# Kernel tuning notes

Hardware: AMD Instinct MI355X
Metric: run time of the kernel (lower is better)

## Reference

```python
import jax, jax.numpy as jnp
import numpy as np

H = 24  # hidden size hard-coded in TrendGRU


def setup_inputs() -> dict:
    key = jax.random.key(0)
    ks = jax.random.split(key, 7)
    B, T = 32768, 512
    s_ih = 1.0 / np.sqrt(H)
    x = jax.random.normal(ks[0], (B, T, 1), dtype=jnp.float32)
    # GRUCell params (PyTorch layout: rows ordered r, z, n)
    W_ih = jax.random.uniform(ks[1], (3 * H, 1), minval=-s_ih, maxval=s_ih, dtype=jnp.float32)
    W_hh = jax.random.uniform(ks[2], (3 * H, H), minval=-s_ih, maxval=s_ih, dtype=jnp.float32)
    b_ih = jax.random.uniform(ks[3], (3 * H,), minval=-s_ih, maxval=s_ih, dtype=jnp.float32)
    b_hh = jax.random.uniform(ks[4], (3 * H,), minval=-s_ih, maxval=s_ih, dtype=jnp.float32)
    fc_w = jax.random.uniform(ks[5], (2, H), minval=-s_ih, maxval=s_ih, dtype=jnp.float32)
    fc_b = jax.random.uniform(ks[6], (2,), minval=-s_ih, maxval=s_ih, dtype=jnp.float32)
    return {"x": x, "W_ih": W_ih, "b_ih": b_ih, "W_hh": W_hh, "b_hh": b_hh,
            "fc_w": fc_w, "fc_b": fc_b}


def _gru_scan(x, W_ih, b_ih, W_hh, b_hh):
    B = x.shape[0]
    # precompute input projections for all timesteps: (B,T,1)@(1,3H) -> (T,B,3H)
    gx = jnp.einsum('bti,gi->tbg', x, W_ih) + b_ih
    h0 = jnp.zeros((B, H), dtype=x.dtype)

    def step(h, gx_t):
        gh = h @ W_hh.T + b_hh                      # (B, 3H)
        xr, xz, xn = jnp.split(gx_t, 3, axis=-1)    # PyTorch order r, z, n
        hr, hz, hn = jnp.split(gh, 3, axis=-1)
        r = jax.nn.sigmoid(xr + hr)
        z = jax.nn.sigmoid(xz + hz)
        n = jnp.tanh(xn + r * hn)
        h_new = (1.0 - z) * n + z * h
        return h_new, None

    h_final, _ = jax.lax.scan(step, h0, gx)
    return h_final


def reference(x, W_ih, b_ih, W_hh, b_hh, fc_w, fc_b):
    h = _gru_scan(x, W_ih, b_ih, W_hh, b_hh)
    return h @ fc_w.T + fc_b  # (B, 2)
```

## Files before the change

kernel.cpp:

```cpp
#include <hip/hip_runtime.h>


#define GRU_T 512
#define FS 28

typedef __attribute__((ext_vector_type(8)))  short bf16x8;
typedef __attribute__((ext_vector_type(16))) float f32x16;
typedef __attribute__((ext_vector_type(2)))  float f32x2;
typedef __attribute__((ext_vector_type(2)))  unsigned uint2v;

__device__ __forceinline__ float bf16hi_f(float v) {
    unsigned u = __float_as_uint(v);
    u = (u + 0x7FFFu + ((u >> 16) & 1u)) & 0xFFFF0000u;
    return __uint_as_float(u);
}
__device__ __forceinline__ unsigned bf16_rne(float v) {
    unsigned u = __float_as_uint(v);
    return (u + 0x7FFFu + ((u >> 16) & 1u)) >> 16;
}
__device__ __forceinline__ unsigned cvt_pk_bf16(float lo, float hi) {
    unsigned r;
    asm("v_cvt_pk_bf16_f32 %0, %1, %2" : "=v"(r) : "v"(lo), "v"(hi));
    return r;
}
__device__ __forceinline__ f32x16 mfma32(bf16x8 a, bf16x8 b, f32x16 c) {
    return __builtin_amdgcn_mfma_f32_32x32x16_bf16(a, b, c, 0, 0, 0);
}

__device__ __forceinline__ unsigned pair_epi(float ar0, float ar1,
                                             float az0, float az1,
                                             float an0, float an1,
                                             const f32x2 aX, f32x2& h)
{
    const f32x2 one2 = {1.0f, 1.0f};
    f32x2 er2, ez2, ev2;
    er2.x = __builtin_amdgcn_exp2f(-ar0);
    er2.y = __builtin_amdgcn_exp2f(-ar1);
    ez2.x = __builtin_amdgcn_exp2f(-az0);
    ez2.y = __builtin_amdgcn_exp2f(-az1);
    const f32x2 dr2 = er2 + one2;
    const f32x2 dz2 = ez2 + one2;
    const f32x2 pp2 = dr2 * dz2;
    const float  Q  = __builtin_amdgcn_rcpf(pp2.x * pp2.y);
    f32x2 qi2; qi2.x = Q * pp2.y; qi2.y = Q * pp2.x;
    const f32x2 rr2 = qi2 * dz2;
    const f32x2 zz2 = qi2 * dr2;
    const f32x2 an2 = {an0, an1};
    const f32x2 u2  = __builtin_elementwise_fma(rr2, an2, aX);
    ev2.x = __builtin_amdgcn_exp2f(u2.x);
    ev2.y = __builtin_amdgcn_exp2f(u2.y);
    const f32x2 dv2 = ev2 + one2;
    const float  Qn = __builtin_amdgcn_rcpf(dv2.x * dv2.y);
    f32x2 rv2; rv2.x = Qn * dv2.y; rv2.y = Qn * dv2.x;
    const f32x2 m2  = {-2.0f, -2.0f};
    const f32x2 nn2 = __builtin_elementwise_fma(m2, rv2, one2);
    const f32x2 hm2 = h - nn2;
    const f32x2 hn2 = __builtin_elementwise_fma(zz2, hm2, nn2);
    h = hn2;
    return cvt_pk_bf16(hn2.x, hn2.y);
}

__global__ __launch_bounds__(64) void trend_gru_mfma32(
    const float* __restrict__ x,
    const float* __restrict__ W_ih,
    const float* __restrict__ b_ih,
    const float* __restrict__ W_hh,
    const float* __restrict__ b_hh,
    const float* __restrict__ fc_w,
    const float* __restrict__ fc_b,
    float* __restrict__ out)
{
    const int lane = threadIdx.x;
    const int e    = lane & 31;
    const int half = lane >> 5;
    const int elem0 = blockIdx.x * 32;

    __shared__ __align__(16) float Flds[32 * FS];

    const float L2E = 1.4426950408889634f;

    bf16x8 A[3][2][2];
#pragma unroll
    for (int g = 0; g < 3; ++g) {
        const float sc = (g == 2) ? 2.0f * L2E : L2E;
        const int m = e;
        const bool valid = m < 24;
        const int R = g * 24 + (valid ? m : 0);
        const float wx = (g < 2 && valid) ? sc * W_ih[R] : 0.0f;
        const float bb = valid ? sc * ((g < 2) ? (b_ih[R] + b_hh[R]) : b_hh[R]) : 0.0f;
        const float wxh = bf16hi_f(wx), bbh = bf16hi_f(bb);
#pragma unroll
        for (int s = 0; s < 2; ++s) {
            bf16x8 fh, fl;
#pragma unroll
            for (int jj = 0; jj < 8; ++jj) {
                const int k = s * 16 + half * 8 + jj;
                float vh = 0.0f, vl = 0.0f;
                if (valid && k < 24) {
                    const float w  = sc * W_hh[R * 24 + k];
                    const float wh = bf16hi_f(w);
                    vh = wh; vl = w - wh;
                } else if (valid) {
                    if (k == 24 || k == 25)      vh = wxh;
                    else if (k == 26)            vh = wx - wxh;
                    else if (k == 27)            vh = bbh;
                    else if (k == 28)            vh = bb - bbh;
                }
                fh[jj] = (short)bf16_rne(vh);
                fl[jj] = (short)bf16_rne(vl);
            }
            A[g][s][0] = fh;
            A[g][s][1] = fl;
        }
    }

    f32x2 wn2[6], bn2[6];
#pragma unroll
    for (int p = 0; p < 6; ++p) {
#pragma unroll
        for (int c = 0; c < 2; ++c) {
            const int s = p * 2 + c;
            const int j = (s & 3) + 8 * (s >> 2) + 4 * half;
            wn2[p][c] = 2.0f * L2E * W_ih[48 + j];
            bn2[p][c] = 2.0f * L2E * b_ih[48 + j];
        }
    }

    const float* xp = x + (size_t)(elem0 + e) * GRU_T;

    f32x2 h2[6];
#pragma unroll
    for (int p = 0; p < 6; ++p) { h2[p].x = 0.0f; h2[p].y = 0.0f; }

    const f32x16 z16 = {0.f,0.f,0.f,0.f,0.f,0.f,0.f,0.f,
                        0.f,0.f,0.f,0.f,0.f,0.f,0.f,0.f};

    float xv    = xp[0];
    float xnext = xp[1];

    f32x2 aX2[6];
#pragma unroll
    for (int p = 0; p < 6; ++p) {
        const f32x2 xb = {xv, xv};
        aX2[p] = __builtin_elementwise_fma(wn2[p], xb, bn2[p]);
    }

    f32x16 aR, aZ, aN;
    {
        uint4 b1q; b1q.x = 0u; b1q.y = 0u; b1q.z = 0u; b1q.w = 0u;
        if (half) {
            const unsigned xy = cvt_pk_bf16(xv, 1.0f);
            const float    xh = __uint_as_float(xy << 16);
            const unsigned xx = cvt_pk_bf16(xv, xv - xh);
            b1q.x = xx; b1q.y = xy; b1q.z = 0x00003F80u; b1q.w = 0u;
        }
        const bf16x8 B1 = *(const bf16x8*)&b1q;
        uint4 b0q; b0q.x = 0u; b0q.y = 0u; b0q.z = 0u; b0q.w = 0u;
        const bf16x8 B0 = *(const bf16x8*)&b0q;
        aR = mfma32(A[0][1][0], B1, mfma32(A[0][1][1], B1, z16));
        aZ = mfma32(A[1][1][0], B1, mfma32(A[1][1][1], B1, z16));
        aN = mfma32(A[2][1][0], B1, mfma32(A[2][1][1], B1, z16));
        aR = mfma32(A[0][0][0], B0, mfma32(A[0][0][1], B0, aR));
        aZ = mfma32(A[1][0][0], B0, mfma32(A[1][0][1], B0, aZ));
        aN = mfma32(A[2][0][0], B0, mfma32(A[2][0][1], B0, aN));
    }

#pragma unroll 1
    for (int t = 0; t < GRU_T - 1; ++t) {
        const unsigned nP4 = pair_epi(aR[8],  aR[9],  aZ[8],  aZ[9],
                                      aN[8],  aN[9],  aX2[4], h2[4]);
        const unsigned nP5 = pair_epi(aR[10], aR[11], aZ[10], aZ[11],
                                      aN[10], aN[11], aX2[5], h2[5]);
        const uint2v r44 = __builtin_amdgcn_permlane32_swap(nP4, nP4, false, false);
        const uint2v r55 = __builtin_amdgcn_permlane32_swap(nP5, nP5, false, false);
        uint4 b1q;
        b1q.x = nP4;
        b1q.y = nP5;
        b1q.z = r44.y;
        b1q.w = r55.y;
        if (half) {
            const unsigned xy = cvt_pk_bf16(xnext, 1.0f);
            const float    xh = __uint_as_float(xy << 16);
            const unsigned xx = cvt_pk_bf16(xnext, xnext - xh);
            b1q.x = xx; b1q.y = xy; b1q.z = 0x00003F80u; b1q.w = 0u;
        }
        const bf16x8 B1 = *(const bf16x8*)&b1q;

        f32x16 nR = mfma32(A[0][1][0], B1, mfma32(A[0][1][1], B1, z16));
        f32x16 nZ = mfma32(A[1][1][0], B1, mfma32(A[1][1][1], B1, z16));
        f32x16 nN = mfma32(A[2][1][0], B1, mfma32(A[2][1][1], B1, z16));

        const unsigned nP0 = pair_epi(aR[0], aR[1], aZ[0], aZ[1],
                                      aN[0], aN[1], aX2[0], h2[0]);
        const unsigned nP1 = pair_epi(aR[2], aR[3], aZ[2], aZ[3],
                                      aN[2], aN[3], aX2[1], h2[1]);
        const unsigned nP2 = pair_epi(aR[4], aR[5], aZ[4], aZ[5],
                                      aN[4], aN[5], aX2[2], h2[2]);
        const unsigned nP3 = pair_epi(aR[6], aR[7], aZ[6], aZ[7],
                                      aN[6], aN[7], aX2[3], h2[3]);
        const uint2v r02 = __builtin_amdgcn_permlane32_swap(nP0, nP2, false, false);
        const uint2v r13 = __builtin_amdgcn_permlane32_swap(nP1, nP3, false, false);
        uint4 b0q;
        b0q.x = r02.x;
        b0q.y = r13.x;
        b0q.z = r02.y;
        b0q.w = r13.y;
        const bf16x8 B0 = *(const bf16x8*)&b0q;

        nR = mfma32(A[0][0][0], B0, mfma32(A[0][0][1], B0, nR));
        nZ = mfma32(A[1][0][0], B0, mfma32(A[1][0][1], B0, nZ));
        nN = mfma32(A[2][0][0], B0, mfma32(A[2][0][1], B0, nN));

        const float xcur = xnext;
        xnext = xp[(t + 2 < GRU_T) ? t + 2 : GRU_T - 1];
#pragma unroll
        for (int p = 0; p < 6; ++p) {
            const f32x2 xb = {xcur, xcur};
            aX2[p] = __builtin_elementwise_fma(wn2[p], xb, bn2[p]);
        }
        aR = nR; aZ = nZ; aN = nN;
    }

    (void)pair_epi(aR[8],  aR[9],  aZ[8],  aZ[9],  aN[8],  aN[9],  aX2[4], h2[4]);
    (void)pair_epi(aR[10], aR[11], aZ[10], aZ[11], aN[10], aN[11], aX2[5], h2[5]);
    (void)pair_epi(aR[0],  aR[1],  aZ[0],  aZ[1],  aN[0],  aN[1],  aX2[0], h2[0]);
    (void)pair_epi(aR[2],  aR[3],  aZ[2],  aZ[3],  aN[2],  aN[3],  aX2[1], h2[1]);
    (void)pair_epi(aR[4],  aR[5],  aZ[4],  aZ[5],  aN[4],  aN[5],  aX2[2], h2[2]);
    (void)pair_epi(aR[6],  aR[7],  aZ[6],  aZ[7],  aN[6],  aN[7],  aX2[3], h2[3]);

#pragma unroll
    for (int G = 0; G < 3; ++G) {
        float4 f4;
        f4.x = h2[G * 2 + 0].x; f4.y = h2[G * 2 + 0].y;
        f4.z = h2[G * 2 + 1].x; f4.w = h2[G * 2 + 1].y;
        *(float4*)(&Flds[e * FS + G * 8 + half * 4]) = f4;
    }
    __builtin_amdgcn_s_barrier();
    if (lane < 32) {
        float o0 = fc_b[0], o1 = fc_b[1];
#pragma unroll
        for (int j = 0; j < 24; ++j) {
            const float hv = Flds[lane * FS + j];
            o0 = fmaf(hv, fc_w[j],      o0);
            o1 = fmaf(hv, fc_w[24 + j], o1);
        }
        float2 o; o.x = o0; o.y = o1;
        *(float2*)(out + (size_t)(elem0 + lane) * 2) = o;
    }
}

extern "C" void kernel_launch(void* const* d_in, const int* in_sizes, int n_in,
                              void* d_out, int out_size, void* d_ws, size_t ws_size,
                              hipStream_t stream) {
    const float* x    = (const float*)d_in[0];
    const float* W_ih = (const float*)d_in[1];
    const float* b_ih = (const float*)d_in[2];
    const float* W_hh = (const float*)d_in[3];
    const float* b_hh = (const float*)d_in[4];
    const float* fc_w = (const float*)d_in[5];
    const float* fc_b = (const float*)d_in[6];
    float* out = (float*)d_out;

    const int B = in_sizes[0] / GRU_T;
    const int grid = B / 32;
    trend_gru_mfma32<<<grid, 64, 0, stream>>>(x, W_ih, b_ih, W_hh, b_hh,
                                              fc_w, fc_b, out);
}
```

Measured before the change: 454.0 us.

## Switch GRU recurrence from 32x32 MFMA to 16x16x32 MFMA with 16 sequences per wave

```diff
diff --git a/kernel.cpp b/kernel.cpp
--- a/kernel.cpp
+++ b/kernel.cpp
@@ -5,9 +5,8 @@
 #define FS 28
 
 typedef __attribute__((ext_vector_type(8)))  short bf16x8;
-typedef __attribute__((ext_vector_type(16))) float f32x16;
+typedef __attribute__((ext_vector_type(4)))  float f32x4;
 typedef __attribute__((ext_vector_type(2)))  float f32x2;
-typedef __attribute__((ext_vector_type(2)))  unsigned uint2v;
 
 __device__ __forceinline__ float bf16hi_f(float v) {
     unsigned u = __float_as_uint(v);
@@ -23,8 +22,8 @@
     asm("v_cvt_pk_bf16_f32 %0, %1, %2" : "=v"(r) : "v"(lo), "v"(hi));
     return r;
 }
-__device__ __forceinline__ f32x16 mfma32(bf16x8 a, bf16x8 b, f32x16 c) {
-    return __builtin_amdgcn_mfma_f32_32x32x16_bf16(a, b, c, 0, 0, 0);
+__device__ __forceinline__ f32x4 mfma16(bf16x8 a, bf16x8 b, f32x4 c) {
+    return __builtin_amdgcn_mfma_f32_16x16x32_bf16(a, b, c, 0, 0, 0);
 }
 
 __device__ __forceinline__ unsigned pair_epi(float ar0, float ar1,
@@ -60,7 +59,7 @@
     return cvt_pk_bf16(hn2.x, hn2.y);
 }
 
-__global__ __launch_bounds__(64) void trend_gru_mfma32(
+__global__ __launch_bounds__(64) void trend_gru_mfma16(
     const float* __restrict__ x,
     const float* __restrict__ W_ih,
     const float* __restrict__ b_ih,
@@ -71,30 +70,30 @@
     float* __restrict__ out)
 {
     const int lane = threadIdx.x;
-    const int e    = lane & 31;
-    const int half = lane >> 5;
-    const int elem0 = blockIdx.x * 32;
-
-    __shared__ __align__(16) float Flds[32 * FS];
+    const int e = lane & 15;
+    const int g = lane >> 4;
+    const int elem0 = blockIdx.x * 16;
+
+    __shared__ __align__(16) float Flds[16 * FS];
 
     const float L2E = 1.4426950408889634f;
 
     bf16x8 A[3][2][2];
 #pragma unroll
-    for (int g = 0; g < 3; ++g) {
-        const float sc = (g == 2) ? 2.0f * L2E : L2E;
-        const int m = e;
-        const bool valid = m < 24;
-        const int R = g * 24 + (valid ? m : 0);
-        const float wx = (g < 2 && valid) ? sc * W_ih[R] : 0.0f;
-        const float bb = valid ? sc * ((g < 2) ? (b_ih[R] + b_hh[R]) : b_hh[R]) : 0.0f;
-        const float wxh = bf16hi_f(wx), bbh = bf16hi_f(bb);
-#pragma unroll
-        for (int s = 0; s < 2; ++s) {
+    for (int gate = 0; gate < 3; ++gate) {
+        const float sc = (gate == 2) ? 2.0f * L2E : L2E;
+#pragma unroll
+        for (int tile = 0; tile < 2; ++tile) {
+            const int m = tile * 16 + e;
+            const bool valid = m < 24;
+            const int R = gate * 24 + (valid ? m : 0);
+            const float wx = (gate < 2 && valid) ? sc * W_ih[R] : 0.0f;
+            const float bb = valid ? sc * ((gate < 2) ? (b_ih[R] + b_hh[R]) : b_hh[R]) : 0.0f;
+            const float wxh = bf16hi_f(wx), bbh = bf16hi_f(bb);
             bf16x8 fh, fl;
 #pragma unroll
-            for (int jj = 0; jj < 8; ++jj) {
-                const int k = s * 16 + half * 8 + jj;
+            for (int i = 0; i < 8; ++i) {
+                const int k = g * 8 + i;
                 float vh = 0.0f, vl = 0.0f;
                 if (valid && k < 24) {
                     const float w  = sc * W_hh[R * 24 + k];
@@ -106,137 +105,105 @@
                     else if (k == 27)            vh = bbh;
                     else if (k == 28)            vh = bb - bbh;
                 }
-                fh[jj] = (short)bf16_rne(vh);
-                fl[jj] = (short)bf16_rne(vl);
+                fh[i] = (short)bf16_rne(vh);
+                fl[i] = (short)bf16_rne(vl);
             }
-            A[g][s][0] = fh;
-            A[g][s][1] = fl;
-        }
-    }
-
-    f32x2 wn2[6], bn2[6];
-#pragma unroll
-    for (int p = 0; p < 6; ++p) {
+            A[gate][tile][0] = fh;
+            A[gate][tile][1] = fl;
+        }
+    }
+
+    f32x2 wn2[4], bn2[4];
+#pragma unroll
+    for (int p = 0; p < 4; ++p) {
 #pragma unroll
         for (int c = 0; c < 2; ++c) {
-            const int s = p * 2 + c;
-            const int j = (s & 3) + 8 * (s >> 2) + 4 * half;
+            int j = (p < 2) ? (4 * g + 2 * p + c) : (16 + 4 * g + 2 * (p - 2) + c);
+            if (j > 23) j = 23;
             wn2[p][c] = 2.0f * L2E * W_ih[48 + j];
             bn2[p][c] = 2.0f * L2E * b_ih[48 + j];
         }
     }
 
     const float* xp = x + (size_t)(elem0 + e) * GRU_T;
-
-    f32x2 h2[6];
-#pragma unroll
-    for (int p = 0; p < 6; ++p) { h2[p].x = 0.0f; h2[p].y = 0.0f; }
-
-    const f32x16 z16 = {0.f,0.f,0.f,0.f,0.f,0.f,0.f,0.f,
-                        0.f,0.f,0.f,0.f,0.f,0.f,0.f,0.f};
-
-    float xv    = xp[0];
-    float xnext = xp[1];
-
-    f32x2 aX2[6];
-#pragma unroll
-    for (int p = 0; p < 6; ++p) {
+    float xv = xp[0];
+
+    f32x2 h2[4];
+#pragma unroll
+    for (int p = 0; p < 4; ++p) { h2[p].x = 0.0f; h2[p].y = 0.0f; }
+
+    f32x2 aX2[4];
+#pragma unroll
+    for (int p = 0; p < 4; ++p) {
         const f32x2 xb = {xv, xv};
         aX2[p] = __builtin_elementwise_fma(wn2[p], xb, bn2[p]);
     }
 
-    f32x16 aR, aZ, aN;
+    unsigned Wd0 = 0, Wd1 = 0, Wd2 = 0, Wd3 = 0;
+
+    const int idxA = (e + ((g & 1) << 5)) << 2;
+    const int idxB = idxA + (16 << 2);
+    const int idxC = e << 2;
+    const int idxD = (e + 16) << 2;
+    const bool mg2 = (g == 2);
+    const bool mg3 = (g == 3);
+
+    const f32x4 z4 = {0.f, 0.f, 0.f, 0.f};
+
+#pragma unroll 1
+    for (int t = 0; t < GRU_T; ++t) {
+        const unsigned xy = cvt_pk_bf16(xv, 1.0f);
+        const float    xh = __uint_as_float(xy << 16);
+        const unsigned xx = cvt_pk_bf16(xv, xv - xh);
+
+        unsigned Bd0 = (unsigned)__builtin_amdgcn_ds_bpermute(idxA, (int)Wd0);
+        unsigned Bd1 = (unsigned)__builtin_amdgcn_ds_bpermute(idxA, (int)Wd1);
+        unsigned Bd2 = (unsigned)__builtin_amdgcn_ds_bpermute(idxB, (int)Wd0);
+        unsigned Bd3 = (unsigned)__builtin_amdgcn_ds_bpermute(idxB, (int)Wd1);
+        const unsigned c0 = (unsigned)__builtin_amdgcn_ds_bpermute(idxC, (int)Wd2);
+        const unsigned c1 = (unsigned)__builtin_amdgcn_ds_bpermute(idxC, (int)Wd3);
+        const unsigned c2 = (unsigned)__builtin_amdgcn_ds_bpermute(idxD, (int)Wd2);
+        const unsigned c3 = (unsigned)__builtin_amdgcn_ds_bpermute(idxD, (int)Wd3);
+        Bd0 = mg2 ? c0 : Bd0;  Bd1 = mg2 ? c1 : Bd1;
+        Bd2 = mg2 ? c2 : Bd2;  Bd3 = mg2 ? c3 : Bd3;
+        Bd0 = mg3 ? xx : Bd0;  Bd1 = mg3 ? xy : Bd1;
+        Bd2 = mg3 ? 0x00003F80u : Bd2;  Bd3 = mg3 ? 0u : Bd3;
+        uint4 bq; bq.x = Bd0; bq.y = Bd1; bq.z = Bd2; bq.w = Bd3;
+        const bf16x8 Bf = *(const bf16x8*)&bq;
+        const float xnext = xp[(t + 1 < GRU_T) ? t + 1 : t];
+
+        f32x4 cR0 = mfma16(A[0][0][0], Bf, z4); cR0 = mfma16(A[0][0][1], Bf, cR0);
+        f32x4 cZ0 = mfma16(A[1][0][0], Bf, z4); cZ0 = mfma16(A[1][0][1], Bf, cZ0);
+        f32x4 cN0 = mfma16(A[2][0][0], Bf, z4); cN0 = mfma16(A[2][0][1], Bf, cN0);
+        f32x4 cR1 = mfma16(A[0][1][0], Bf, z4); cR1 = mfma16(A[0][1][1], Bf, cR1);
+        f32x4 cZ1 = mfma16(A[1][1][0], Bf, z4); cZ1 = mfma16(A[1][1][1], Bf, cZ1);
+        f32x4 cN1 = mfma16(A[2][1][0], Bf, z4); cN1 = mfma16(A[2][1][1], Bf, cN1);
+
+        Wd0 = pair_epi(cR0[0], cR0[1], cZ0[0], cZ0[1], cN0[0], cN0[1], aX2[0], h2[0]);
+        Wd1 = pair_epi(cR0[2], cR0[3], cZ0[2], cZ0[3], cN0[2], cN0[3], aX2[1], h2[1]);
+        Wd2 = pair_epi(cR1[0], cR1[1], cZ1[0], cZ1[1], cN1[0], cN1[1], aX2[2], h2[2]);
+        Wd3 = pair_epi(cR1[2], cR1[3], cZ1[2], cZ1[3], cN1[2], cN1[3], aX2[3], h2[3]);
+
+        xv = xnext;
+#pragma unroll
+        for (int p = 0; p < 4; ++p) {
+            const f32x2 xb = {xv, xv};
+            aX2[p] = __builtin_elementwise_fma(wn2[p], xb, bn2[p]);
+        }
+    }
+
     {
-        uint4 b1q; b1q.x = 0u; b1q.y = 0u; b1q.z = 0u; b1q.w = 0u;
-        if (half) {
-            const unsigned xy = cvt_pk_bf16(xv, 1.0f);
-            const float    xh = __uint_as_float(xy << 16);
-            const unsigned xx = cvt_pk_bf16(xv, xv - xh);
-            b1q.x = xx; b1q.y = xy; b1q.z = 0x00003F80u; b1q.w = 0u;
-        }
-        const bf16x8 B1 = *(const bf16x8*)&b1q;
-        uint4 b0q; b0q.x = 0u; b0q.y = 0u; b0q.z = 0u; b0q.w = 0u;
-        const bf16x8 B0 = *(const bf16x8*)&b0q;
-        aR = mfma32(A[0][1][0], B1, mfma32(A[0][1][1], B1, z16));
-        aZ = mfma32(A[1][1][0], B1, mfma32(A[1][1][1], B1, z16));
-        aN = mfma32(A[2][1][0], B1, mfma32(A[2][1][1], B1, z16));
-        aR = mfma32(A[0][0][0], B0, mfma32(A[0][0][1], B0, aR));
-        aZ = mfma32(A[1][0][0], B0, mfma32(A[1][0][1], B0, aZ));
-        aN = mfma32(A[2][0][0], B0, mfma32(A[2][0][1], B0, aN));
-    }
-
-#pragma unroll 1
-    for (int t = 0; t < GRU_T - 1; ++t) {
-        const unsigned nP4 = pair_epi(aR[8],  aR[9],  aZ[8],  aZ[9],
-                                      aN[8],  aN[9],  aX2[4], h2[4]);
-        const unsigned nP5 = pair_epi(aR[10], aR[11], aZ[10], aZ[11],
-                                      aN[10], aN[11], aX2[5], h2[5]);
-        const uint2v r44 = __builtin_amdgcn_permlane32_swap(nP4, nP4, false, false);
-        const uint2v r55 = __builtin_amdgcn_permlane32_swap(nP5, nP5, false, false);
-        uint4 b1q;
-        b1q.x = nP4;
-        b1q.y = nP5;
-        b1q.z = r44.y;
-        b1q.w = r55.y;
-        if (half) {
-            const unsigned xy = cvt_pk_bf16(xnext, 1.0f);
-            const float    xh = __uint_as_float(xy << 16);
-            const unsigned xx = cvt_pk_bf16(xnext, xnext - xh);
-            b1q.x = xx; b1q.y = xy; b1q.z = 0x00003F80u; b1q.w = 0u;
-        }
-        const bf16x8 B1 = *(const bf16x8*)&b1q;
-
-        f32x16 nR = mfma32(A[0][1][0], B1, mfma32(A[0][1][1], B1, z16));
-        f32x16 nZ = mfma32(A[1][1][0], B1, mfma32(A[1][1][1], B1, z16));
-        f32x16 nN = mfma32(A[2][1][0], B1, mfma32(A[2][1][1], B1, z16));
-
-        const unsigned nP0 = pair_epi(aR[0], aR[1], aZ[0], aZ[1],
-                                      aN[0], aN[1], aX2[0], h2[0]);
-        const unsigned nP1 = pair_epi(aR[2], aR[3], aZ[2], aZ[3],
-                                      aN[2], aN[3], aX2[1], h2[1]);
-        const unsigned nP2 = pair_epi(aR[4], aR[5], aZ[4], aZ[5],
-                                      aN[4], aN[5], aX2[2], h2[2]);
-        const unsigned nP3 = pair_epi(aR[6], aR[7], aZ[6], aZ[7],
-                                      aN[6], aN[7], aX2[3], h2[3]);
-        const uint2v r02 = __builtin_amdgcn_permlane32_swap(nP0, nP2, false, false);
-        const uint2v r13 = __builtin_amdgcn_permlane32_swap(nP1, nP3, false, false);
-        uint4 b0q;
-        b0q.x = r02.x;
-        b0q.y = r13.x;
-        b0q.z = r02.y;
-        b0q.w = r13.y;
-        const bf16x8 B0 = *(const bf16x8*)&b0q;
-
-        nR = mfma32(A[0][0][0], B0, mfma32(A[0][0][1], B0, nR));
-        nZ = mfma32(A[1][0][0], B0, mfma32(A[1][0][1], B0, nZ));
-        nN = mfma32(A[2][0][0], B0, mfma32(A[2][0][1], B0, nN));
-
-        const float xcur = xnext;
-        xnext = xp[(t + 2 < GRU_T) ? t + 2 : GRU_T - 1];
-#pragma unroll
-        for (int p = 0; p < 6; ++p) {
-            const f32x2 xb = {xcur, xcur};
-            aX2[p] = __builtin_elementwise_fma(wn2[p], xb, bn2[p]);
-        }
-        aR = nR; aZ = nZ; aN = nN;
-    }
-
-    (void)pair_epi(aR[8],  aR[9],  aZ[8],  aZ[9],  aN[8],  aN[9],  aX2[4], h2[4]);
-    (void)pair_epi(aR[10], aR[11], aZ[10], aZ[11], aN[10], aN[11], aX2[5], h2[5]);
-    (void)pair_epi(aR[0],  aR[1],  aZ[0],  aZ[1],  aN[0],  aN[1],  aX2[0], h2[0]);
-    (void)pair_epi(aR[2],  aR[3],  aZ[2],  aZ[3],  aN[2],  aN[3],  aX2[1], h2[1]);
-    (void)pair_epi(aR[4],  aR[5],  aZ[4],  aZ[5],  aN[4],  aN[5],  aX2[2], h2[2]);
-    (void)pair_epi(aR[6],  aR[7],  aZ[6],  aZ[7],  aN[6],  aN[7],  aX2[3], h2[3]);
-
-#pragma unroll
-    for (int G = 0; G < 3; ++G) {
         float4 f4;
-        f4.x = h2[G * 2 + 0].x; f4.y = h2[G * 2 + 0].y;
-        f4.z = h2[G * 2 + 1].x; f4.w = h2[G * 2 + 1].y;
-        *(float4*)(&Flds[e * FS + G * 8 + half * 4]) = f4;
+        f4.x = h2[0].x; f4.y = h2[0].y; f4.z = h2[1].x; f4.w = h2[1].y;
+        *(float4*)(&Flds[e * FS + 4 * g]) = f4;
+        if (g < 2) {
+            float4 f5;
+            f5.x = h2[2].x; f5.y = h2[2].y; f5.z = h2[3].x; f5.w = h2[3].y;
+            *(float4*)(&Flds[e * FS + 16 + 4 * g]) = f5;
+        }
     }
     __builtin_amdgcn_s_barrier();
-    if (lane < 32) {
+    if (lane < 16) {
         float o0 = fc_b[0], o1 = fc_b[1];
 #pragma unroll
         for (int j = 0; j < 24; ++j) {
@@ -262,7 +229,7 @@
     float* out = (float*)d_out;
 
     const int B = in_sizes[0] / GRU_T;
-    const int grid = B / 32;
-    trend_gru_mfma32<<<grid, 64, 0, stream>>>(x, W_ih, b_ih, W_hh, b_hh,
+    const int grid = B / 16;
+    trend_gru_mfma16<<<grid, 64, 0, stream>>>(x, W_ih, b_ih, W_hh, b_hh,
                                               fc_w, fc_b, out);
 }
```

Result: slower. 514.5 us (+13.3%).

## Interleave two independent GRU sequences per wave to hide MFMA latency

Applied to the files above, without the earlier changes.

```diff
diff --git a/kernel.cpp b/kernel.cpp
--- a/kernel.cpp
+++ b/kernel.cpp
@@ -60,7 +60,7 @@
     return cvt_pk_bf16(hn2.x, hn2.y);
 }
 
-__global__ __launch_bounds__(64) void trend_gru_mfma32(
+__global__ __launch_bounds__(64, 1) void trend_gru_dual(
     const float* __restrict__ x,
     const float* __restrict__ W_ih,
     const float* __restrict__ b_ih,
@@ -73,9 +73,9 @@
     const int lane = threadIdx.x;
     const int e    = lane & 31;
     const int half = lane >> 5;
-    const int elem0 = blockIdx.x * 32;
-
-    __shared__ __align__(16) float Flds[32 * FS];
+    const int elem0 = blockIdx.x * 64;
+
+    __shared__ __align__(16) float Flds[2 * 32 * FS];
 
     const float L2E = 1.4426950408889634f;
 
@@ -126,126 +126,169 @@
         }
     }
 
-    const float* xp = x + (size_t)(elem0 + e) * GRU_T;
-
-    f32x2 h2[6];
-#pragma unroll
-    for (int p = 0; p < 6; ++p) { h2[p].x = 0.0f; h2[p].y = 0.0f; }
+    const float* xpa = x + (size_t)(elem0 + e) * GRU_T;
+    const float* xpb = xpa + (size_t)32 * GRU_T;
+
+    f32x2 h2a[6], h2b[6];
+#pragma unroll
+    for (int p = 0; p < 6; ++p) {
+        h2a[p].x = 0.0f; h2a[p].y = 0.0f;
+        h2b[p].x = 0.0f; h2b[p].y = 0.0f;
+    }
+    unsigned Pa0 = 0, Pa1 = 0, Pa2 = 0, Pa3 = 0, Pa4 = 0, Pa5 = 0;
+    unsigned Pb0 = 0, Pb1 = 0, Pb2 = 0, Pb3 = 0, Pb4 = 0, Pb5 = 0;
+
+    float xva = xpa[0];
+    float xvb = xpb[0];
+
+    f32x2 aX2a[6], aX2b[6];
+#pragma unroll
+    for (int p = 0; p < 6; ++p) {
+        const f32x2 xa = {xva, xva};
+        const f32x2 xb = {xvb, xvb};
+        aX2a[p] = __builtin_elementwise_fma(wn2[p], xa, bn2[p]);
+        aX2b[p] = __builtin_elementwise_fma(wn2[p], xb, bn2[p]);
+    }
 
     const f32x16 z16 = {0.f,0.f,0.f,0.f,0.f,0.f,0.f,0.f,
                         0.f,0.f,0.f,0.f,0.f,0.f,0.f,0.f};
 
-    float xv    = xp[0];
-    float xnext = xp[1];
-
-    f32x2 aX2[6];
-#pragma unroll
-    for (int p = 0; p < 6; ++p) {
-        const f32x2 xb = {xv, xv};
-        aX2[p] = __builtin_elementwise_fma(wn2[p], xb, bn2[p]);
-    }
-
-    f32x16 aR, aZ, aN;
-    {
-        uint4 b1q; b1q.x = 0u; b1q.y = 0u; b1q.z = 0u; b1q.w = 0u;
+#pragma unroll 1
+    for (int t = 0; t < GRU_T; ++t) {
+        const uint2v ra02 = __builtin_amdgcn_permlane32_swap(Pa0, Pa2, false, false);
+        const uint2v ra13 = __builtin_amdgcn_permlane32_swap(Pa1, Pa3, false, false);
+        uint4 b0qa;
+        b0qa.x = ra02.x; b0qa.y = ra13.x; b0qa.z = ra02.y; b0qa.w = ra13.y;
+        const uint2v ra44 = __builtin_amdgcn_permlane32_swap(Pa4, Pa4, false, false);
+        const uint2v ra55 = __builtin_amdgcn_permlane32_swap(Pa5, Pa5, false, false);
+        uint4 b1qa;
+        b1qa.x = Pa4; b1qa.y = Pa5; b1qa.z = ra44.y; b1qa.w = ra55.y;
         if (half) {
-            const unsigned xy = cvt_pk_bf16(xv, 1.0f);
+            const unsigned xy = cvt_pk_bf16(xva, 1.0f);
             const float    xh = __uint_as_float(xy << 16);
-            const unsigned xx = cvt_pk_bf16(xv, xv - xh);
-            b1q.x = xx; b1q.y = xy; b1q.z = 0x00003F80u; b1q.w = 0u;
-        }
-        const bf16x8 B1 = *(const bf16x8*)&b1q;
-        uint4 b0q; b0q.x = 0u; b0q.y = 0u; b0q.z = 0u; b0q.w = 0u;
-        const bf16x8 B0 = *(const bf16x8*)&b0q;
-        aR = mfma32(A[0][1][0], B1, mfma32(A[0][1][1], B1, z16));
-        aZ = mfma32(A[1][1][0], B1, mfma32(A[1][1][1], B1, z16));
-        aN = mfma32(A[2][1][0], B1, mfma32(A[2][1][1], B1, z16));
-        aR = mfma32(A[0][0][0], B0, mfma32(A[0][0][1], B0, aR));
-        aZ = mfma32(A[1][0][0], B0, mfma32(A[1][0][1], B0, aZ));
-        aN = mfma32(A[2][0][0], B0, mfma32(A[2][0][1], B0, aN));
-    }
-
-#pragma unroll 1
-    for (int t = 0; t < GRU_T - 1; ++t) {
-        const unsigned nP4 = pair_epi(aR[8],  aR[9],  aZ[8],  aZ[9],
-                                      aN[8],  aN[9],  aX2[4], h2[4]);
-        const unsigned nP5 = pair_epi(aR[10], aR[11], aZ[10], aZ[11],
-                                      aN[10], aN[11], aX2[5], h2[5]);
-        const uint2v r44 = __builtin_amdgcn_permlane32_swap(nP4, nP4, false, false);
-        const uint2v r55 = __builtin_amdgcn_permlane32_swap(nP5, nP5, false, false);
-        uint4 b1q;
-        b1q.x = nP4;
-        b1q.y = nP5;
-        b1q.z = r44.y;
-        b1q.w = r55.y;
+            const unsigned xx = cvt_pk_bf16(xva, xva - xh);
+            b1qa.x = xx; b1qa.y = xy; b1qa.z = 0x00003F80u; b1qa.w = 0u;
+        }
+        const bf16x8 B0a = *(const bf16x8*)&b0qa;
+        const bf16x8 B1a = *(const bf16x8*)&b1qa;
+        const float xnexta = xpa[(t + 1 < GRU_T) ? t + 1 : t];
+
+        f32x16 aRa = mfma32(A[0][0][0], B0a, z16);
+        aRa = mfma32(A[0][0][1], B0a, aRa);
+        aRa = mfma32(A[0][1][0], B1a, aRa);
+        aRa = mfma32(A[0][1][1], B1a, aRa);
+        f32x16 aZa = mfma32(A[1][0][0], B0a, z16);
+        aZa = mfma32(A[1][0][1], B0a, aZa);
+        aZa = mfma32(A[1][1][0], B1a, aZa);
+        aZa = mfma32(A[1][1][1], B1a, aZa);
+        f32x16 aNa = mfma32(A[2][0][0], B0a, z16);
+        aNa = mfma32(A[2][0][1], B0a, aNa);
+        aNa = mfma32(A[2][1][0], B1a, aNa);
+        aNa = mfma32(A[2][1][1], B1a, aNa);
+
+        const uint2v rb02 = __builtin_amdgcn_permlane32_swap(Pb0, Pb2, false, false);
+        const uint2v rb13 = __builtin_amdgcn_permlane32_swap(Pb1, Pb3, false, false);
+        uint4 b0qb;
+        b0qb.x = rb02.x; b0qb.y = rb13.x; b0qb.z = rb02.y; b0qb.w = rb13.y;
+        const uint2v rb44 = __builtin_amdgcn_permlane32_swap(Pb4, Pb4, false, false);
+        const uint2v rb55 = __builtin_amdgcn_permlane32_swap(Pb5, Pb5, false, false);
+        uint4 b1qb;
+        b1qb.x = Pb4; b1qb.y = Pb5; b1qb.z = rb44.y; b1qb.w = rb55.y;
         if (half) {
-            const unsigned xy = cvt_pk_bf16(xnext, 1.0f);
+            const unsigned xy = cvt_pk_bf16(xvb, 1.0f);
             const float    xh = __uint_as_float(xy << 16);
-            const unsigned xx = cvt_pk_bf16(xnext, xnext - xh);
-            b1q.x = xx; b1q.y = xy; b1q.z = 0x00003F80u; b1q.w = 0u;
-        }
-        const bf16x8 B1 = *(const bf16x8*)&b1q;
-
-        f32x16 nR = mfma32(A[0][1][0], B1, mfma32(A[0][1][1], B1, z16));
-        f32x16 nZ = mfma32(A[1][1][0], B1, mfma32(A[1][1][1], B1, z16));
-        f32x16 nN = mfma32(A[2][1][0], B1, mfma32(A[2][1][1], B1, z16));
-
-        const unsigned nP0 = pair_epi(aR[0], aR[1], aZ[0], aZ[1],
-                                      aN[0], aN[1], aX2[0], h2[0]);
-        const unsigned nP1 = pair_epi(aR[2], aR[3], aZ[2], aZ[3],
-                                      aN[2], aN[3], aX2[1], h2[1]);
-        const unsigned nP2 = pair_epi(aR[4], aR[5], aZ[4], aZ[5],
-                                      aN[4], aN[5], aX2[2], h2[2]);
-        const unsigned nP3 = pair_epi(aR[6], aR[7], aZ[6], aZ[7],
-                                      aN[6], aN[7], aX2[3], h2[3]);
-        const uint2v r02 = __builtin_amdgcn_permlane32_swap(nP0, nP2, false, false);
-        const uint2v r13 = __builtin_amdgcn_permlane32_swap(nP1, nP3, false, false);
-        uint4 b0q;
-        b0q.x = r02.x;
-        b0q.y = r13.x;
-        b0q.z = r02.y;
-        b0q.w = r13.y;
-        const bf16x8 B0 = *(const bf16x8*)&b0q;
-
-        nR = mfma32(A[0][0][0], B0, mfma32(A[0][0][1], B0, nR));
-        nZ = mfma32(A[1][0][0], B0, mfma32(A[1][0][1], B0, nZ));
-        nN = mfma32(A[2][0][0], B0, mfma32(A[2][0][1], B0, nN));
-
-        const float xcur = xnext;
-        xnext = xp[(t + 2 < GRU_T) ? t + 2 : GRU_T - 1];
+            const unsigned xx = cvt_pk_bf16(xvb, xvb - xh);
+            b1qb.x = xx; b1qb.y = xy; b1qb.z = 0x00003F80u; b1qb.w = 0u;
+        }
+        const bf16x8 B0b = *(const bf16x8*)&b0qb;
+        const bf16x8 B1b = *(const bf16x8*)&b1qb;
+        const float xnextb = xpb[(t + 1 < GRU_T) ? t + 1 : t];
+
+        f32x16 aRb = mfma32(A[0][0][0], B0b, z16);
+        aRb = mfma32(A[0][0][1], B0b, aRb);
+        aRb = mfma32(A[0][1][0], B1b, aRb);
+        aRb = mfma32(A[0][1][1], B1b, aRb);
+        f32x16 aZb = mfma32(A[1][0][0], B0b, z16);
+        aZb = mfma32(A[1][0][1], B0b, aZb);
+        aZb = mfma32(A[1][1][0], B1b, aZb);
+        aZb = mfma32(A[1][1][1], B1b, aZb);
+        f32x16 aNb = mfma32(A[2][0][0], B0b, z16);
+        aNb = mfma32(A[2][0][1], B0b, aNb);
+        aNb = mfma32(A[2][1][0], B1b, aNb);
+        aNb = mfma32(A[2][1][1], B1b, aNb);
+
+#pragma unroll
+        for (int G = 0; G < 3; ++G) {
+            const unsigned pa = pair_epi(aRa[G*4+0], aRa[G*4+1],
+                                         aZa[G*4+0], aZa[G*4+1],
+                                         aNa[G*4+0], aNa[G*4+1],
+                                         aX2a[G*2], h2a[G*2]);
+            const unsigned pb = pair_epi(aRa[G*4+2], aRa[G*4+3],
+                                         aZa[G*4+2], aZa[G*4+3],
+                                         aNa[G*4+2], aNa[G*4+3],
+                                         aX2a[G*2+1], h2a[G*2+1]);
+            if (G == 0)      { Pa0 = pa; Pa1 = pb; }
+            else if (G == 1) { Pa2 = pa; Pa3 = pb; }
+            else             { Pa4 = pa; Pa5 = pb; }
+        }
+        xva = xnexta;
 #pragma unroll
         for (int p = 0; p < 6; ++p) {
-            const f32x2 xb = {xcur, xcur};
-            aX2[p] = __builtin_elementwise_fma(wn2[p], xb, bn2[p]);
-        }
-        aR = nR; aZ = nZ; aN = nN;
-    }
-
-    (void)pair_epi(aR[8],  aR[9],  aZ[8],  aZ[9],  aN[8],  aN[9],  aX2[4], h2[4]);
-    (void)pair_epi(aR[10], aR[11], aZ[10], aZ[11], aN[10], aN[11], aX2[5], h2[5]);
-    (void)pair_epi(aR[0],  aR[1],  aZ[0],  aZ[1],  aN[0],  aN[1],  aX2[0], h2[0]);
-    (void)pair_epi(aR[2],  aR[3],  aZ[2],  aZ[3],  aN[2],  aN[3],  aX2[1], h2[1]);
-    (void)pair_epi(aR[4],  aR[5],  aZ[4],  aZ[5],  aN[4],  aN[5],  aX2[2], h2[2]);
-    (void)pair_epi(aR[6],  aR[7],  aZ[6],  aZ[7],  aN[6],  aN[7],  aX2[3], h2[3]);
-
+            const f32x2 xa = {xva, xva};
+            aX2a[p] = __builtin_elementwise_fma(wn2[p], xa, bn2[p]);
+        }
+
+#pragma unroll
+        for (int G = 0; G < 3; ++G) {
+            const unsigned pa = pair_epi(aRb[G*4+0], aRb[G*4+1],
+                                         aZb[G*4+0], aZb[G*4+1],
+                                         aNb[G*4+0], aNb[G*4+1],
+                                         aX2b[G*2], h2b[G*2]);
+            const unsigned pb = pair_epi(aRb[G*4+2], aRb[G*4+3],
+                                         aZb[G*4+2], aZb[G*4+3],
+                                         aNb[G*4+2], aNb[G*4+3],
+                                         aX2b[G*2+1], h2b[G*2+1]);
+            if (G == 0)      { Pb0 = pa; Pb1 = pb; }
+            else if (G == 1) { Pb2 = pa; Pb3 = pb; }
+            else             { Pb4 = pa; Pb5 = pb; }
+        }
+        xvb = xnextb;
+#pragma unroll
+        for (int p = 0; p < 6; ++p) {
+            const f32x2 xb = {xvb, xvb};
+            aX2b[p] = __builtin_elementwise_fma(wn2[p], xb, bn2[p]);
+        }
+    }
+
+    float* Fa = Flds;
+    float* Fb = Flds + 32 * FS;
 #pragma unroll
     for (int G = 0; G < 3; ++G) {
         float4 f4;
-        f4.x = h2[G * 2 + 0].x; f4.y = h2[G * 2 + 0].y;
-        f4.z = h2[G * 2 + 1].x; f4.w = h2[G * 2 + 1].y;
-        *(float4*)(&Flds[e * FS + G * 8 + half * 4]) = f4;
-    }
-    __builtin_amdgcn_s_barrier();
+        f4.x = h2a[G * 2 + 0].x; f4.y = h2a[G * 2 + 0].y;
+        f4.z = h2a[G * 2 + 1].x; f4.w = h2a[G * 2 + 1].y;
+        *(float4*)(&Fa[e * FS + G * 8 + half * 4]) = f4;
+        float4 f5;
+        f5.x = h2b[G * 2 + 0].x; f5.y = h2b[G * 2 + 0].y;
+        f5.z = h2b[G * 2 + 1].x; f5.w = h2b[G * 2 + 1].y;
+        *(float4*)(&Fb[e * FS + G * 8 + half * 4]) = f5;
+    }
     if (lane < 32) {
         float o0 = fc_b[0], o1 = fc_b[1];
+        float q0 = fc_b[0], q1 = fc_b[1];
 #pragma unroll
         for (int j = 0; j < 24; ++j) {
-            const float hv = Flds[lane * FS + j];
-            o0 = fmaf(hv, fc_w[j],      o0);
-            o1 = fmaf(hv, fc_w[24 + j], o1);
-        }
-        float2 o; o.x = o0; o.y = o1;
-        *(float2*)(out + (size_t)(elem0 + lane) * 2) = o;
+            const float ha = Fa[lane * FS + j];
+            const float hb = Fb[lane * FS + j];
+            o0 = fmaf(ha, fc_w[j],      o0);
+            o1 = fmaf(ha, fc_w[24 + j], o1);
+            q0 = fmaf(hb, fc_w[j],      q0);
+            q1 = fmaf(hb, fc_w[24 + j], q1);
+        }
+        float2 oa; oa.x = o0; oa.y = o1;
+        float2 ob; ob.x = q0; ob.y = q1;
+        *(float2*)(out + (size_t)(elem0 + lane) * 2) = oa;
+        *(float2*)(out + (size_t)(elem0 + 32 + lane) * 2) = ob;
     }
 }
 
@@ -262,7 +305,7 @@
     float* out = (float*)d_out;
 
     const int B = in_sizes[0] / GRU_T;
-    const int grid = B / 32;
-    trend_gru_mfma32<<<grid, 64, 0, stream>>>(x, W_ih, b_ih, W_hh, b_hh,
-                                              fc_w, fc_b, out);
-}
+    const int grid = B / 64;
+    trend_gru_dual<<<grid, 64, 0, stream>>>(x, W_ih, b_ih, W_hh, b_hh,
+                                            fc_w, fc_b, out);
+}
```

Measured after the change: 739.8 us. 62.9% more time.
